# Performance work log

Measured on AMD Instinct MI355X. Metric: run time of the kernel, lower is better.

Reference implementation:

```python
import jax, jax.numpy as jnp
import numpy as np

EPS = 1e-6
NEG = -10000.0

def compute_alibi_slopes(n_head):
    # standard ALiBi slopes for power-of-two head counts: 2^{-8(i+1)/n}
    start = 2.0 ** (-8.0 / n_head)
    return jnp.asarray([start ** (i + 1) for i in range(n_head)], dtype=jnp.float32)

def setup_inputs() -> dict:
    key = jax.random.key(0)
    k1, k2, k3 = jax.random.split(key, 3)
    B, T, C, H = 2, 2048, 1024, 16
    x = jax.random.normal(k1, (B, T, C), dtype=jnp.float32)
    # torch nn.Linear weights are [out_features, in_features]
    w_qkv = jax.random.normal(k2, (3 * C, C), dtype=jnp.float32) * (C ** -0.5)
    w_out = jax.random.normal(k3, (C, C), dtype=jnp.float32) * (C ** -0.5)
    alibi_slopes = compute_alibi_slopes(H)
    return {"x": x, "w_qkv": w_qkv, "w_out": w_out, "alibi_slopes": alibi_slopes}

def rational_softmax(scores, eps=EPS):
    # algebraic sigmoid 0.5*(1 + x/sqrt(1+x^2)) normalized along last axis
    num = 0.5 * (1.0 + scores * jax.lax.rsqrt(1.0 + scores * scores))
    return num / (jnp.sum(num, axis=-1, keepdims=True) + eps)

def reference(x, w_qkv, w_out, alibi_slopes):
    B, T, C = x.shape
    H = alibi_slopes.shape[0]
    D = C // H
    scale = 1.0 / jnp.sqrt(jnp.float32(D))
    qkv = (x @ w_qkv.T).reshape(B, T, 3, H, D)
    qkv = jnp.transpose(qkv, (2, 0, 3, 1, 4))  # [3,B,H,T,D]
    q, k, v = qkv[0], qkv[1], qkv[2]
    scores = jnp.einsum("bhtd,bhsd->bhts", q, k) * scale  # [B,H,T,T]
    pos = jnp.arange(T)
    rel = pos[:, None] - pos[None, :]  # [T,T]
    alibi = -jnp.abs(rel).astype(jnp.float32) * alibi_slopes[None, :, None, None]
    scores = scores + alibi
    causal = rel < 0  # strictly upper triangle (j > i)
    scores = jnp.where(causal[None, None], NEG, scores)
    probs = rational_softmax(scores, EPS)
    out = jnp.einsum("bhts,bhsd->bhtd", probs, v)  # [B,H,T,D]
    out = jnp.transpose(out, (0, 2, 1, 3)).reshape(B, T, C)
    return out @ w_out.T
```

## Files before the change

### kernel.cpp

```cpp
#include <hip/hip_runtime.h>
#include <stdint.h>

typedef __attribute__((ext_vector_type(8))) short bf16x8;
typedef __attribute__((ext_vector_type(4))) float f32x4;
typedef __attribute__((ext_vector_type(16))) float f32x16;

#define MFMA_16x16x32(a, b, c) __builtin_amdgcn_mfma_f32_16x16x32_bf16((a), (b), (c), 0, 0, 0)
#define MFMA_32x32x16(a, b, c) __builtin_amdgcn_mfma_f32_32x32x16_bf16((a), (b), (c), 0, 0, 0)

__device__ __forceinline__ short f2bf(float f) {
  union { float f; uint32_t u; } x;
  x.f = f;
  uint32_t r = x.u + 0x7fffu + ((x.u >> 16) & 1u);
  return (short)(r >> 16);
}

__device__ __forceinline__ uint32_t cvt_pk_bf16(float lo, float hi) {
  uint32_t r;
  asm("v_cvt_pk_bf16_f32 %0, %1, %2" : "=v"(r) : "v"(lo), "v"(hi));
  return r;
}

__device__ __forceinline__ void gload_lds16(const short* g, short* l) {
  __builtin_amdgcn_global_load_lds(
      (const __attribute__((address_space(1))) void*)g,
      (__attribute__((address_space(3))) void*)l, 16, 0, 0);
}

__global__ __launch_bounds__(256) void cast_all(const float* __restrict__ x,
                                                const float* __restrict__ wq,
                                                const float* __restrict__ wo,
                                                short* __restrict__ xb,
                                                short* __restrict__ wqb,
                                                short* __restrict__ wob) {
  int i = blockIdx.x * 256 + threadIdx.x;
  const float* s;
  short* d;
  int off;
  float sc = 1.0f;
  if (i < 524288) { s = x; d = xb; off = i; }
  else if (i < 917504) {
    s = wq; d = wqb; off = i - 524288;
    if (off < 131072) sc = 0.125f;
  }
  else { s = wo; d = wob; off = i - 917504; }
  const float4* sp = (const float4*)s;
  float4 v0 = sp[(size_t)off * 2 + 0];
  float4 v1 = sp[(size_t)off * 2 + 1];
  bf16x8 o;
  o[0] = f2bf(v0.x * sc); o[1] = f2bf(v0.y * sc); o[2] = f2bf(v0.z * sc); o[3] = f2bf(v0.w * sc);
  o[4] = f2bf(v1.x * sc); o[5] = f2bf(v1.y * sc); o[6] = f2bf(v1.z * sc); o[7] = f2bf(v1.w * sc);
  *(bf16x8*)(d + (size_t)off * 8) = o;
}

template <int OUT_BF16>
__global__ __launch_bounds__(512, 2) void gemm256(const short* __restrict__ A,
                                                  const short* __restrict__ B,
                                                  void* __restrict__ Cp,
                                                  int M, int N, int K, int ntN) {
  __shared__ short Al[2][2][128 * 64];
  __shared__ short Bl[2][3][64 * 64];

  const int tid = threadIdx.x;
  const int wv = tid >> 6, lane = tid & 63;
  const int wr = wv >> 2, wc = wv & 3;
  const int lrow = lane & 15, kgrp = lane >> 4;
  const int l3 = lrow & 7;
  const int ck0 = ((kgrp ^ l3)) * 8;
  const int ck1 = ((kgrp ^ l3) ^ 4) * 8;

  const int nwg = gridDim.x;
  const int orig = blockIdx.x;
  const int wg = (orig & 7) * (nwg >> 3) + (orig >> 3);
  const int by = wg / ntN, bx = wg % ntN;
  const int row0 = by * 256, col0 = bx * 192;

  const int r_ = tid >> 3;
  const int cs_ = ((tid & 7) ^ (r_ & 7)) * 8;

  const int NT = K >> 6;
  const int NI = NT >> 1;
  const int NTm1 = NT - 1;

  auto stgA = [&](int slot, int h, int j, int kt) {
    gload_lds16(A + (size_t)(row0 + h * 128 + j * 64 + r_) * K + kt * 64 + cs_,
                &Al[slot][h][j * 4096 + wv * 512]);
  };
  auto stgB = [&](int slot, int j, int kt) {
    gload_lds16(B + (size_t)(col0 + j * 64 + r_) * K + kt * 64 + cs_,
                &Bl[slot][j][wv * 512]);
  };

  f32x4 acc[8][3] = {};

  stgB(0, 0, 0); stgB(0, 1, 0); stgB(0, 2, 0);
  stgA(0, 0, 0, 0); stgA(0, 0, 1, 0); stgA(0, 1, 0, 0); stgA(0, 1, 1, 0);
  stgB(1, 0, 1); stgB(1, 1, 1); stgB(1, 2, 1);
  asm volatile("s_waitcnt vmcnt(3)" ::: "memory");
  __builtin_amdgcn_s_barrier();

  for (int i = 0; i < NI; ++i) {
    const int ktB1 = (2 * i + 1);
    const int ktP2 = (2 * i + 2 > NTm1) ? NTm1 : 2 * i + 2;
    const int ktP3 = (2 * i + 3 > NTm1) ? NTm1 : 2 * i + 3;
#pragma unroll
    for (int s = 0; s < 2; ++s) {
      bf16x8 bfr[3][2];
#pragma unroll
      for (int q = 0; q < 4; ++q) {
        if (q == 0) {
#pragma unroll
          for (int n = 0; n < 3; ++n) {
            const int row = wc * 48 + n * 16 + lrow;
            const int th = row >> 6;
            const int lr = row & 63;
            bfr[n][0] = *(const bf16x8*)(&Bl[s][th][lr * 64 + ck0]);
            bfr[n][1] = *(const bf16x8*)(&Bl[s][th][lr * 64 + ck1]);
          }
        }
        bf16x8 afr[2][2];
#pragma unroll
        for (int mm = 0; mm < 2; ++mm) {
          const int m = q * 2 + mm;
          afr[mm][0] = *(const bf16x8*)(&Al[s][wr][lrow * 64 + m * 1024 + ck0]);
          afr[mm][1] = *(const bf16x8*)(&Al[s][wr][lrow * 64 + m * 1024 + ck1]);
        }
        if (s == 0) {
          if (q == 0) { stgA(1, 0, 0, ktB1); stgA(1, 0, 1, ktB1); stgA(1, 1, 0, ktB1); stgA(1, 1, 1, ktB1); }
          else if (q == 1) { stgB(0, 0, ktP2); stgB(0, 1, ktP2); }
          else if (q == 2) { stgB(0, 2, ktP2); }
        } else {
          if (q == 0) { stgA(0, 0, 0, ktP2); stgA(0, 0, 1, ktP2); stgA(0, 1, 0, ktP2); stgA(0, 1, 1, ktP2); }
          else if (q == 1) { stgB(1, 0, ktP3); stgB(1, 1, ktP3); }
          else if (q == 2) { stgB(1, 2, ktP3); }
        }
        __builtin_amdgcn_sched_barrier(0);
        __builtin_amdgcn_s_barrier();
        asm volatile("s_waitcnt lgkmcnt(0)" ::: "memory");
        __builtin_amdgcn_sched_barrier(0);
        __builtin_amdgcn_s_setprio(1);
#pragma unroll
        for (int mm = 0; mm < 2; ++mm)
#pragma unroll
          for (int n = 0; n < 3; ++n)
#pragma unroll
            for (int kk = 0; kk < 2; ++kk)
              acc[q * 2 + mm][n] = MFMA_16x16x32(afr[mm][kk], bfr[n][kk], acc[q * 2 + mm][n]);
        __builtin_amdgcn_s_setprio(0);
        __builtin_amdgcn_sched_barrier(0);
        if (q == 3) {
          asm volatile("s_waitcnt vmcnt(3)" ::: "memory");
        }
        __builtin_amdgcn_s_barrier();
      }
    }
  }

  asm volatile("s_waitcnt vmcnt(0)" ::: "memory");

#pragma unroll
  for (int m = 0; m < 8; ++m) {
    const int grow = row0 + wr * 128 + m * 16 + kgrp * 4;
#pragma unroll
    for (int n = 0; n < 3; ++n) {
      const int gcol = col0 + wc * 48 + n * 16 + lrow;
#pragma unroll
      for (int j = 0; j < 4; ++j) {
        const size_t off = (size_t)(grow + j) * N + gcol;
        if (OUT_BF16) ((short*)Cp)[off] = f2bf(acc[m][n][j]);
        else          ((float*)Cp)[off] = acc[m][n][j];
      }
    }
  }
}

template <int OUT_BF16>
__global__ __launch_bounds__(256, 4) void gemm_bt64(const short* __restrict__ A,
                                                    const short* __restrict__ B,
                                                    void* __restrict__ Cp,
                                                    int M, int N, int K) {
  __shared__ short As[2][64 * 64];
  __shared__ short Bs[2][128 * 64];
  const int tid = threadIdx.x;
  const int wave = tid >> 6, lane = tid & 63;
  const int wr = wave >> 1, wc = wave & 1;
  const int row0 = blockIdx.y * 64, col0 = blockIdx.x * 128;
  const int lrow = lane & 15;
  const int kgrp = lane >> 4;
  const int l3 = lrow & 7;

  const int r_ = tid >> 3;
  const int cs_ = ((tid & 7) ^ (r_ & 7)) * 8;

  const int NT = K >> 6;

  auto STG = [&](int buf, int kt) {
#pragma unroll
    for (int it = 0; it < 2; ++it)
      gload_lds16(A + (size_t)(row0 + it * 32 + r_) * K + kt * 64 + cs_,
                  &As[buf][(it * 256 + wave * 64) * 8]);
#pragma unroll
    for (int it = 0; it < 4; ++it)
      gload_lds16(B + (size_t)(col0 + it * 32 + r_) * K + kt * 64 + cs_,
                  &Bs[buf][(it * 256 + wave * 64) * 8]);
  };

  f32x4 acc[2][4] = {};

  STG(0, 0);

  for (int kt = 0; kt < NT; ++kt) {
    __builtin_amdgcn_s_barrier();
    __builtin_amdgcn_sched_barrier(0);
    const int ktn = (kt + 1 >= NT) ? NT - 1 : kt + 1;
    STG((kt + 1) & 1, ktn);
    asm volatile("s_waitcnt vmcnt(6)" ::: "memory");
    __builtin_amdgcn_sched_barrier(0);
    const short* Ab = As[kt & 1];
    const short* Bb = Bs[kt & 1];
#pragma unroll
    for (int kk = 0; kk < 2; ++kk) {
      const int ck = ((kk * 4 + kgrp) ^ l3) * 8;
      bf16x8 a[2], b[4];
#pragma unroll
      for (int m = 0; m < 2; ++m)
        a[m] = *(const bf16x8*)(Ab + (wr * 32 + m * 16 + lrow) * 64 + ck);
#pragma unroll
      for (int n = 0; n < 4; ++n)
        b[n] = *(const bf16x8*)(Bb + (wc * 64 + n * 16 + lrow) * 64 + ck);
#pragma unroll
      for (int m = 0; m < 2; ++m)
#pragma unroll
        for (int n = 0; n < 4; ++n)
          acc[m][n] = MFMA_16x16x32(a[m], b[n], acc[m][n]);
    }
  }

  asm volatile("s_waitcnt vmcnt(0)" ::: "memory");

#pragma unroll
  for (int m = 0; m < 2; ++m) {
    int rbase = row0 + wr * 32 + m * 16 + kgrp * 4;
#pragma unroll
    for (int n = 0; n < 4; ++n) {
      int col = col0 + wc * 64 + n * 16 + lrow;
#pragma unroll
      for (int j = 0; j < 4; ++j) {
        size_t off = (size_t)(rbase + j) * N + col;
        if (OUT_BF16) ((short*)Cp)[off] = f2bf(acc[m][n][j]);
        else          ((float*)Cp)[off] = acc[m][n][j];
      }
    }
  }
}

__global__ __launch_bounds__(256) void transpose_v(const short* __restrict__ qkv,
                                                   short* __restrict__ vt) {
  const int T = 2048;
  __shared__ short sm[64][72];
  const int bh = blockIdx.y, h = bh & 15, b = bh >> 4;
  const int t0 = blockIdx.x * 64;
  const int tid = threadIdx.x;
#pragma unroll
  for (int p = 0; p < 2; ++p) {
    int idx = p * 256 + tid;
    int tl = idx >> 3, d0 = (idx & 7) * 8;
    bf16x8 v = *(const bf16x8*)(qkv + (b * T + t0 + tl) * 3072 + 2048 + h * 64 + d0);
    *(bf16x8*)(&sm[tl][d0]) = v;
  }
  __syncthreads();
#pragma unroll
  for (int p = 0; p < 2; ++p) {
    int idx = p * 256 + tid;
    int d = idx >> 3, ts0 = (idx & 7) * 8;
    bf16x8 o;
#pragma unroll
    for (int j = 0; j < 8; ++j) o[j] = sm[ts0 + j][d];
    *(bf16x8*)(vt + (bh * 64 + d) * T + t0 + ts0) = o;
  }
}

template <bool DIAG>
__device__ __forceinline__ void attn_sub(
    const short* __restrict__ Kb, const short* __restrict__ Vb,
    const bf16x8 (&qf)[4], const f32x16& crun,
    f32x16& acc0, f32x16& acc1, float (&den4)[4],
    int l31, int hi, int shalf, int mbits) {
  const int krow = l31 >> 1;
  const int kc0 = (l31 & 1) * 8 + hi;
  const int ss = shalf;
  const bf16x8 kf0 = *(const bf16x8*)(Kb + (ss * 16 + krow) * 128 + ((kc0 + 0) ^ krow) * 8);
  const bf16x8 kf1 = *(const bf16x8*)(Kb + (ss * 16 + krow) * 128 + ((kc0 + 2) ^ krow) * 8);
  const bf16x8 kf2 = *(const bf16x8*)(Kb + (ss * 16 + krow) * 128 + ((kc0 + 4) ^ krow) * 8);
  const bf16x8 kf3 = *(const bf16x8*)(Kb + (ss * 16 + krow) * 128 + ((kc0 + 6) ^ krow) * 8);
  __builtin_amdgcn_s_setprio(1);
  f32x16 zz = {};
  f32x16 sA = MFMA_32x32x16(kf0, qf[0], crun);
  f32x16 sB = MFMA_32x32x16(kf2, qf[2], zz);
  sA = MFMA_32x32x16(kf1, qf[1], sA);
  sB = MFMA_32x32x16(kf3, qf[3], sB);
  __builtin_amdgcn_s_setprio(0);
  float nm[16];
#pragma unroll
  for (int v = 0; v < 16; ++v) {
    float x = sA[v] + sB[v];
    if (DIAG) x = ((mbits >> v) & 1) ? -10000.0f : x;
    float t = fmaf(x, x, 1.0f);
    float num = fmaf(x * __builtin_amdgcn_rsqf(t), 0.5f, 0.5f);
    den4[v & 3] += num;
    nm[v] = num;
  }
#pragma unroll
  for (int k1 = 0; k1 < 2; ++k1) {
    union { uint32_t u[4]; bf16x8 v8; } pu;
#pragma unroll
    for (int w01 = 0; w01 < 2; ++w01) {
      uint32_t c0 = cvt_pk_bf16(nm[2 * w01 + 8 * k1], nm[2 * w01 + 8 * k1 + 1]);
      uint32_t c1 = cvt_pk_bf16(nm[2 * w01 + 8 * k1 + 4], nm[2 * w01 + 8 * k1 + 5]);
      asm volatile("v_permlane32_swap_b32 %0, %1" : "+v"(c0), "+v"(c1));
      pu.u[w01] = c0;
      pu.u[w01 + 2] = c1;
    }
    const int vsw = ((((l31 & 1) * 8) + ss * 4 + k1 * 2 + hi) ^ krow) * 8;
    const bf16x8 vf0 = *(const bf16x8*)(Vb + krow * 128 + vsw);
    const bf16x8 vf1 = *(const bf16x8*)(Vb + (16 + krow) * 128 + vsw);
    __builtin_amdgcn_s_setprio(1);
    acc0 = MFMA_32x32x16(pu.v8, vf0, acc0);
    acc1 = MFMA_32x32x16(pu.v8, vf1, acc1);
    __builtin_amdgcn_s_setprio(0);
  }
}

__device__ __constant__ int HPAIR[8][2] = {
  {15, 0}, {14, 1}, {13, 2}, {12, 3}, {11, 4}, {10, 5}, {9, 6}, {8, 7}};

__global__ __launch_bounds__(256, 3) void attn_kernel(const short* __restrict__ qkv,
                                                      const short* __restrict__ vt,
                                                      const float* __restrict__ slopes,
                                                      short* __restrict__ attn_out) {
  const int T = 2048, C = 1024, C3 = 3072;
  __shared__ short Kl[3][4096];
  __shared__ short Vl[3][4096];
  __shared__ float denm[64];

  const int tid = threadIdx.x, wv = tid >> 6, lane = tid & 63;
  const int l31 = lane & 31, hi = lane >> 5;
  const int wg = blockIdx.x;
  const int xcd = wg & 7, j = wg >> 3;
  const int bhsel = j & 3;
  const int qi = 31 - (j >> 2);
  const int h = HPAIR[xcd][bhsel & 1];
  const int b = bhsel >> 1;
  const int bh = b * 16 + h;
  const int qsub = wv >> 1, shalf = wv & 1;
  const float slope = slopes[h];
  const float s64 = slope * 64.0f;

  const int W = (int)(32.0f / (64.0f * slope)) + 2;
  const int kt0 = (qi - W > 0) ? (qi - W) : 0;

  int mbits = 0;
#pragma unroll
  for (int v = 0; v < 16; ++v) {
    int s32 = (v & 3) + 8 * (v >> 2) + 4 * hi;
    if (s32 > l31) mbits |= (1 << v);
  }
  int koff[2], voff[2];
#pragma unroll
  for (int p = 0; p < 2; ++p) {
    int idx = p * 256 + tid;
    int rho = idx >> 4, u = idx & 15, c = u ^ (rho & 15);
    koff[p] = (2 * rho + (c >> 3)) * C3 + (c & 7) * 8;
    voff[p] = (2 * rho + (c >> 3)) * T + (c & 7) * 8;
  }
  const short* kbase = qkv + (size_t)b * T * C3 + C + h * 64;
  const short* vbase = vt + (size_t)bh * 64 * T;

  auto STAGE = [&](int bufi, int kt) {
#pragma unroll
    for (int p = 0; p < 2; ++p)
      gload_lds16(kbase + (size_t)kt * 64 * C3 + koff[p], &Kl[bufi][(p * 256 + wv * 64) * 8]);
#pragma unroll
    for (int p = 0; p < 2; ++p)
      gload_lds16(vbase + kt * 64 + voff[p], &Vl[bufi][(p * 256 + wv * 64) * 8]);
  };

  const int qg = qi * 64 + qsub * 32 + l31;
  bf16x8 qf[4];
#pragma unroll
  for (int ks = 0; ks < 4; ++ks)
    qf[ks] = *(const bf16x8*)(qkv + (size_t)(b * T + qg) * C3 + h * 64 + ks * 16 + hi * 8);
  __builtin_amdgcn_sched_barrier(0);

  STAGE(0, kt0);
  STAGE(1, (kt0 + 1 > qi) ? qi : kt0 + 1);

  f32x16 crun;
#pragma unroll
  for (int v = 0; v < 16; ++v) {
    int s32 = (v & 3) + 8 * (v >> 2) + 4 * hi;
    crun[v] = slope * (float)(s32 - l31 + 32 * (shalf - qsub) + 64 * (kt0 - qi));
  }

  f32x16 acc0 = {}, acc1 = {};
  float den4[4] = {0.f, 0.f, 0.f, 0.f};

  int cA = 0;
  for (int kt = kt0; kt < qi; ++kt) {
    asm volatile("s_waitcnt vmcnt(4)" ::: "memory");
    __builtin_amdgcn_s_barrier();
    __builtin_amdgcn_sched_barrier(0);
    int cS = cA + 2; if (cS >= 3) cS -= 3;
    STAGE(cS, (kt + 2 > qi) ? qi : kt + 2);
    attn_sub<false>(Kl[cA], Vl[cA], qf, crun, acc0, acc1, den4, l31, hi, shalf, mbits);
#pragma unroll
    for (int v = 0; v < 16; ++v) crun[v] += s64;
    cA = (cA == 2) ? 0 : cA + 1;
  }
  asm volatile("s_waitcnt vmcnt(4)" ::: "memory");
  __builtin_amdgcn_s_barrier();
  if (!(qsub == 0 && shalf == 1)) {
    if (qsub == 1 && shalf == 0)
      attn_sub<false>(Kl[cA], Vl[cA], qf, crun, acc0, acc1, den4, l31, hi, shalf, mbits);
    else
      attn_sub<true>(Kl[cA], Vl[cA], qf, crun, acc0, acc1, den4, l31, hi, shalf, mbits);
  }
  __syncthreads();

  int sc = cA + 1; if (sc >= 3) sc -= 3;
  float den = (den4[0] + den4[1]) + (den4[2] + den4[3]);
  den += __shfl_xor(den, 32);

  if (shalf == 1) {
    float* mp = (float*)(qsub == 0 ? &Kl[sc][0] : &Vl[sc][0]);
#pragma unroll
    for (int i = 0; i < 16; ++i) {
      mp[i * 64 + lane] = acc0[i];
      mp[(16 + i) * 64 + lane] = acc1[i];
    }
    if (hi == 0) denm[qsub * 32 + l31] = den;
  }
  __syncthreads();

  if (shalf == 0) {
    const float* mp = (const float*)(qsub == 0 ? &Kl[sc][0] : &Vl[sc][0]);
    den += denm[qsub * 32 + l31];
#pragma unroll
    for (int i = 0; i < 16; ++i) {
      acc0[i] += mp[i * 64 + lane];
      acc1[i] += mp[(16 + i) * 64 + lane];
    }
    short* obase = attn_out + (size_t)(b * T + qi * 64 + qsub * 32) * C + h * 64;
#pragma unroll
    for (int v = 0; v < 16; ++v) {
      int ql = (v & 3) + 8 * (v >> 2) + 4 * hi;
      float dv = __int_as_float(__builtin_amdgcn_ds_bpermute(ql << 2, __float_as_int(den)));
      float r = __builtin_amdgcn_rcpf(dv + 1e-6f);
      obase[(size_t)ql * C + l31] = f2bf(acc0[v] * r);
      obase[(size_t)ql * C + 32 + l31] = f2bf(acc1[v] * r);
    }
  }
}

extern "C" void kernel_launch(void* const* d_in, const int* in_sizes, int n_in,
                              void* d_out, int out_size, void* d_ws, size_t ws_size,
                              hipStream_t stream) {
  const float* x      = (const float*)d_in[0];
  const float* w_qkv  = (const float*)d_in[1];
  const float* w_out  = (const float*)d_in[2];
  const float* slopes = (const float*)d_in[3];

  const int B = 2, T = 2048, C = 1024;
  const int M = B * T;
  const int N1 = 3 * C;

  char* ws = (char*)d_ws;
  short* x_bf    = (short*)(ws);
  short* wqkv_bf = (short*)(ws + 8388608);
  short* wout_bf = (short*)(ws + 14680064);
  short* qkv_bf  = (short*)(ws + 16777216);
  short* vt_bf   = (short*)(ws + 41943040);
  short* ao_bf   = (short*)(ws + 50331648);

  cast_all<<<4096, 256, 0, stream>>>(x, w_qkv, w_out, x_bf, wqkv_bf, wout_bf);

  gemm256<1><<<dim3((M / 256) * (N1 / 192)), 512, 0, stream>>>(x_bf, wqkv_bf, qkv_bf,
                                                               M, N1, C, N1 / 192);

  transpose_v<<<dim3(T / 64, 32), 256, 0, stream>>>(qkv_bf, vt_bf);

  attn_kernel<<<1024, 256, 0, stream>>>(qkv_bf, vt_bf, slopes, ao_bf);

  gemm_bt64<0><<<dim3(C / 128, M / 64), 256, 0, stream>>>(ao_bf, wout_bf, (float*)d_out, M, C, C);
}
```

Before: 99.89 us.

## Split long key ranges of low-slope heads across two workgroups with merge kernel

The attention grid becomes a 2D launch with one column per XCD that pairs head 15-x and head x. For heads 9-15, whose ALiBi window is long, the 15 highest query tiles have their key range split in half between two workgroups. Each half writes unnormalized fp32 partial sums and denominators to workspace, and a new merge kernel adds them and normalizes to bf16. The aim is to balance per-workgroup load and shorten the critical path, at the cost of an extra launch and partial-buffer traffic that reuses the x_bf workspace region.

```diff
diff --git a/kernel.cpp b/kernel.cpp
--- a/kernel.cpp
+++ b/kernel.cpp
@@ -331,13 +331,11 @@
   }
 }
 
-__device__ __constant__ int HPAIR[8][2] = {
-  {15, 0}, {14, 1}, {13, 2}, {12, 3}, {11, 4}, {10, 5}, {9, 6}, {8, 7}};
-
 __global__ __launch_bounds__(256, 3) void attn_kernel(const short* __restrict__ qkv,
                                                       const short* __restrict__ vt,
                                                       const float* __restrict__ slopes,
-                                                      short* __restrict__ attn_out) {
+                                                      short* __restrict__ attn_out,
+                                                      float* __restrict__ partials) {
   const int T = 2048, C = 1024, C3 = 3072;
   __shared__ short Kl[3][4096];
   __shared__ short Vl[3][4096];
@@ -345,19 +343,43 @@
 
   const int tid = threadIdx.x, wv = tid >> 6, lane = tid & 63;
   const int l31 = lane & 31, hi = lane >> 5;
-  const int wg = blockIdx.x;
-  const int xcd = wg & 7, j = wg >> 3;
-  const int bhsel = j & 3;
-  const int qi = 31 - (j >> 2);
-  const int h = HPAIR[xcd][bhsel & 1];
-  const int b = bhsel >> 1;
+  const int xcd = blockIdx.x;
+  const int by = blockIdx.y;
+  const int hA = 15 - xcd;
+  const int nSplit = (hA >= 9) ? 15 : 0;
+  const int itemsA = 32 + nSplit;
+  const int totA = 2 * itemsA;
+  if (by >= totA + 64) return;
+
+  int h, b, qi, part = -1;
+  if (by < totA) {
+    h = hA; b = by & 1;
+    const int i = by >> 1;
+    if (i < 2 * nSplit) { qi = 31 - (i >> 1); part = i & 1; }
+    else { qi = 31 - nSplit - (i - 2 * nSplit); }
+  } else {
+    const int k = by - totA;
+    h = xcd; b = k & 1; qi = 31 - (k >> 1);
+  }
   const int bh = b * 16 + h;
   const int qsub = wv >> 1, shalf = wv & 1;
   const float slope = slopes[h];
   const float s64 = slope * 64.0f;
 
-  const int W = (int)(32.0f / (64.0f * slope)) + 2;
-  const int kt0 = (qi - W > 0) ? (qi - W) : 0;
+  int W = (int)(32.0f / (64.0f * slope)) + 2;
+  if (W > 31) W = 31;
+  const int kt0f = (qi - W > 0) ? (qi - W) : 0;
+
+  int ktA, ktLim;
+  bool hasdiag;
+  if (part < 0) { ktA = kt0f; ktLim = qi; hasdiag = true; }
+  else {
+    const int L = qi - kt0f + 1;
+    const int nh = (L + 1) >> 1;
+    if (part == 0) { ktA = kt0f; ktLim = kt0f + nh; hasdiag = false; }
+    else           { ktA = kt0f + nh; ktLim = qi; hasdiag = true; }
+  }
+  const int ktMax = hasdiag ? qi : (ktLim - 1);
 
   int mbits = 0;
 #pragma unroll
@@ -392,38 +414,40 @@
     qf[ks] = *(const bf16x8*)(qkv + (size_t)(b * T + qg) * C3 + h * 64 + ks * 16 + hi * 8);
   __builtin_amdgcn_sched_barrier(0);
 
-  STAGE(0, kt0);
-  STAGE(1, (kt0 + 1 > qi) ? qi : kt0 + 1);
+  STAGE(0, ktA);
+  STAGE(1, (ktA + 1 > ktMax) ? ktMax : ktA + 1);
 
   f32x16 crun;
 #pragma unroll
   for (int v = 0; v < 16; ++v) {
     int s32 = (v & 3) + 8 * (v >> 2) + 4 * hi;
-    crun[v] = slope * (float)(s32 - l31 + 32 * (shalf - qsub) + 64 * (kt0 - qi));
+    crun[v] = slope * (float)(s32 - l31 + 32 * (shalf - qsub) + 64 * (ktA - qi));
   }
 
   f32x16 acc0 = {}, acc1 = {};
   float den4[4] = {0.f, 0.f, 0.f, 0.f};
 
   int cA = 0;
-  for (int kt = kt0; kt < qi; ++kt) {
+  for (int kt = ktA; kt < ktLim; ++kt) {
     asm volatile("s_waitcnt vmcnt(4)" ::: "memory");
     __builtin_amdgcn_s_barrier();
     __builtin_amdgcn_sched_barrier(0);
     int cS = cA + 2; if (cS >= 3) cS -= 3;
-    STAGE(cS, (kt + 2 > qi) ? qi : kt + 2);
+    STAGE(cS, (kt + 2 > ktMax) ? ktMax : kt + 2);
     attn_sub<false>(Kl[cA], Vl[cA], qf, crun, acc0, acc1, den4, l31, hi, shalf, mbits);
 #pragma unroll
     for (int v = 0; v < 16; ++v) crun[v] += s64;
     cA = (cA == 2) ? 0 : cA + 1;
   }
-  asm volatile("s_waitcnt vmcnt(4)" ::: "memory");
-  __builtin_amdgcn_s_barrier();
-  if (!(qsub == 0 && shalf == 1)) {
-    if (qsub == 1 && shalf == 0)
-      attn_sub<false>(Kl[cA], Vl[cA], qf, crun, acc0, acc1, den4, l31, hi, shalf, mbits);
-    else
-      attn_sub<true>(Kl[cA], Vl[cA], qf, crun, acc0, acc1, den4, l31, hi, shalf, mbits);
+  if (hasdiag) {
+    asm volatile("s_waitcnt vmcnt(4)" ::: "memory");
+    __builtin_amdgcn_s_barrier();
+    if (!(qsub == 0 && shalf == 1)) {
+      if (qsub == 1 && shalf == 0)
+        attn_sub<false>(Kl[cA], Vl[cA], qf, crun, acc0, acc1, den4, l31, hi, shalf, mbits);
+      else
+        attn_sub<true>(Kl[cA], Vl[cA], qf, crun, acc0, acc1, den4, l31, hi, shalf, mbits);
+    }
   }
   __syncthreads();
 
@@ -450,16 +474,55 @@
       acc0[i] += mp[i * 64 + lane];
       acc1[i] += mp[(16 + i) * 64 + lane];
     }
-    short* obase = attn_out + (size_t)(b * T + qi * 64 + qsub * 32) * C + h * 64;
-#pragma unroll
-    for (int v = 0; v < 16; ++v) {
-      int ql = (v & 3) + 8 * (v >> 2) + 4 * hi;
-      float dv = __int_as_float(__builtin_amdgcn_ds_bpermute(ql << 2, __float_as_int(den)));
-      float r = __builtin_amdgcn_rcpf(dv + 1e-6f);
-      obase[(size_t)ql * C + l31] = f2bf(acc0[v] * r);
-      obase[(size_t)ql * C + 32 + l31] = f2bf(acc1[v] * r);
-    }
-  }
+    if (part < 0) {
+      short* obase = attn_out + (size_t)(b * T + qi * 64 + qsub * 32) * C + h * 64;
+#pragma unroll
+      for (int v = 0; v < 16; ++v) {
+        int ql = (v & 3) + 8 * (v >> 2) + 4 * hi;
+        float dv = __int_as_float(__builtin_amdgcn_ds_bpermute(ql << 2, __float_as_int(den)));
+        float r = __builtin_amdgcn_rcpf(dv + 1e-6f);
+        obase[(size_t)ql * C + l31] = f2bf(acc0[v] * r);
+        obase[(size_t)ql * C + 32 + l31] = f2bf(acc1[v] * r);
+      }
+    } else {
+      const int slot = (b * 7 + (h - 9)) * 15 + (qi - 17);
+      float* pb = partials + (size_t)slot * 8320 + part * 4160;
+#pragma unroll
+      for (int v = 0; v < 16; ++v) {
+        int ql = (v & 3) + 8 * (v >> 2) + 4 * hi;
+        int row = qsub * 32 + ql;
+        pb[row * 64 + l31] = acc0[v];
+        pb[row * 64 + 32 + l31] = acc1[v];
+      }
+      if (hi == 0) pb[4096 + qsub * 32 + l31] = den;
+    }
+  }
+}
+
+__global__ __launch_bounds__(256) void attn_merge(const float* __restrict__ partials,
+                                                  short* __restrict__ attn_out) {
+  const int s = blockIdx.x;
+  const int b = s / 105, r = s % 105;
+  const int h = 9 + r / 15, qi = 17 + r % 15;
+  const float* p0 = partials + (size_t)s * 8320;
+  const float* p1 = p0 + 4160;
+  const int t = threadIdx.x;
+  const int row = t >> 2, g = (t & 3) * 16;
+  const float d = p0[4096 + row] + p1[4096 + row] + 1e-6f;
+  const float rd = __builtin_amdgcn_rcpf(d);
+  short o[16];
+#pragma unroll
+  for (int i = 0; i < 16; i += 4) {
+    float4 a = *(const float4*)(p0 + row * 64 + g + i);
+    float4 c = *(const float4*)(p1 + row * 64 + g + i);
+    o[i + 0] = f2bf((a.x + c.x) * rd);
+    o[i + 1] = f2bf((a.y + c.y) * rd);
+    o[i + 2] = f2bf((a.z + c.z) * rd);
+    o[i + 3] = f2bf((a.w + c.w) * rd);
+  }
+  short* ob = attn_out + ((size_t)(b * 2048 + qi * 64 + row) * 1024 + h * 64 + g);
+  *(bf16x8*)ob = *(bf16x8*)&o[0];
+  *(bf16x8*)(ob + 8) = *(bf16x8*)&o[8];
 }
 
 extern "C" void kernel_launch(void* const* d_in, const int* in_sizes, int n_in,
@@ -481,6 +544,7 @@
   short* qkv_bf  = (short*)(ws + 16777216);
   short* vt_bf   = (short*)(ws + 41943040);
   short* ao_bf   = (short*)(ws + 50331648);
+  float* partials = (float*)(ws);
 
   cast_all<<<4096, 256, 0, stream>>>(x, w_qkv, w_out, x_bf, wqkv_bf, wout_bf);
 
@@ -489,7 +553,9 @@
 
   transpose_v<<<dim3(T / 64, 32), 256, 0, stream>>>(qkv_bf, vt_bf);
 
-  attn_kernel<<<1024, 256, 0, stream>>>(qkv_bf, vt_bf, slopes, ao_bf);
+  attn_kernel<<<dim3(8, 158), 256, 0, stream>>>(qkv_bf, vt_bf, slopes, ao_bf, partials);
+
+  attn_merge<<<210, 256, 0, stream>>>(partials, ao_bf);
 
   gemm_bt64<0><<<dim3(C / 128, M / 64), 256, 0, stream>>>(ao_bf, wout_bf, (float*)d_out, M, C, C);
 }
```

New measurement: 96.51 us. 1.03x faster.
